# Kernel optimization log

Hardware: AMD Instinct MI355X
Metric: run time of the kernel (lower is better)

Reference implementation:

```python
import jax, jax.numpy as jnp
import numpy as np


def setup_inputs() -> dict:
    key = jax.random.key(0)
    k1, k2 = jax.random.split(key)
    B, S, H = 32, 4096, 1024
    output = jax.random.normal(k1, (B, 1, H), dtype=jnp.float32)
    context = jax.random.normal(k2, (B, S, H), dtype=jnp.float32)
    return {"output": output, "context": context}


def reference(output, context):
    # scores: (B, 1, S) = q @ k^T
    attn = jnp.einsum('bqh,bsh->bqs', output, context)
    attn = jax.nn.softmax(attn, axis=2)
    # out: (B, 1, H) = attn @ context, then tanh
    out = jnp.tanh(jnp.einsum('bqs,bsh->bqh', attn, context))
    return (out, attn)
```

## Files before the change

kernel.cpp:

```cpp
#include <hip/hip_runtime.h>
#include <math.h>

constexpr int kB  = 32;
constexpr int kS  = 4096;
constexpr int kH  = 1024;
constexpr int kNC = 128;
constexpr int kCH = kS / kNC;
constexpr int WPB = 4;
constexpr int NP  = kCH / 2;

#define GLOAD_LDS16(gp, lp)                                                        \
  __builtin_amdgcn_global_load_lds(                                               \
      (const __attribute__((address_space(1))) void*)(gp),                        \
      (__attribute__((address_space(3))) void*)(lp), 16, 0, 0)

__device__ __forceinline__ void stage_row(const float* __restrict__ g,
                                          float* l, int lane) {
  #pragma unroll
  for (int j = 0; j < 4; ++j)
    GLOAD_LDS16(g + j * 256 + 4 * lane, l + j * 256);
}

#define PAIR4(acc4, w04, w14) \
  acc4.x = fmaf(p1, w14.x, fmaf(p0, w04.x, acc4.x * sc)); \
  acc4.y = fmaf(p1, w14.y, fmaf(p0, w04.y, acc4.y * sc)); \
  acc4.z = fmaf(p1, w14.z, fmaf(p0, w04.z, acc4.z * sc)); \
  acc4.w = fmaf(p1, w14.w, fmaf(p0, w04.w, acc4.w * sc));

__global__ __launch_bounds__(256, 2) void attn_pass1(
    const float* __restrict__ q,
    const float* __restrict__ ctx,
    float* __restrict__ scores,
    float* __restrict__ pm,
    float* __restrict__ pl,
    float* __restrict__ pacc)
{
  __shared__ __align__(16) float lds[WPB * 2 * 2048];

  const int lane = threadIdx.x & 63;
  const int wid  = threadIdx.x >> 6;
  const int wave = blockIdx.x * WPB + wid;
  const int b    = wave / kNC;
  const int c    = wave % kNC;

  float* wbuf = &lds[wid * 4096];

  const float4* qp = reinterpret_cast<const float4*>(q + (size_t)b * kH) + lane;
  const float4 Qa = qp[0], Qb = qp[64], Qc = qp[128], Qd = qp[192];

  const float* cbase = ctx + ((size_t)b * kS + (size_t)c * kCH) * kH;

  float m = -3.0e38f, l = 0.0f;
  float4 aa = make_float4(0.f,0.f,0.f,0.f), ab = aa, ac = aa, ad = aa;
  float myscore = 0.0f;

  stage_row(cbase,        wbuf,        lane);
  stage_row(cbase + 1024, wbuf + 1024, lane);

  auto compute_pair = [&](int t) {
    const float4* p0 = reinterpret_cast<const float4*>(wbuf + (t & 1) * 2048) + lane;
    const float4* p1 = p0 + 256;

    const float4 w0a = p0[0], w0b = p0[64], w0c = p0[128], w0d = p0[192];
    const float4 w1a = p1[0], w1b = p1[64], w1c = p1[128], w1d = p1[192];

    float d0, d1;
    d0  = w0a.x*Qa.x + w0a.y*Qa.y + w0a.z*Qa.z + w0a.w*Qa.w;
    d0 += w0b.x*Qb.x + w0b.y*Qb.y + w0b.z*Qb.z + w0b.w*Qb.w;
    d0 += w0c.x*Qc.x + w0c.y*Qc.y + w0c.z*Qc.z + w0c.w*Qc.w;
    d0 += w0d.x*Qd.x + w0d.y*Qd.y + w0d.z*Qd.z + w0d.w*Qd.w;
    d1  = w1a.x*Qa.x + w1a.y*Qa.y + w1a.z*Qa.z + w1a.w*Qa.w;
    d1 += w1b.x*Qb.x + w1b.y*Qb.y + w1b.z*Qb.z + w1b.w*Qb.w;
    d1 += w1c.x*Qc.x + w1c.y*Qc.y + w1c.z*Qc.z + w1c.w*Qc.w;
    d1 += w1d.x*Qd.x + w1d.y*Qd.y + w1d.z*Qd.z + w1d.w*Qd.w;

    #pragma unroll
    for (int off = 32; off >= 1; off >>= 1) {
      d0 += __shfl_xor(d0, off, 64);
      d1 += __shfl_xor(d1, off, 64);
    }

    if (lane == 2 * t)     myscore = d0;
    if (lane == 2 * t + 1) myscore = d1;

    const float nm = fmaxf(m, fmaxf(d0, d1));
    const float sc = __expf(m - nm);
    const float p0s = __expf(d0 - nm);
    const float p1s = __expf(d1 - nm);
    m = nm;
    l = fmaf(l, sc, p0s + p1s);
    { const float p0 = p0s, p1 = p1s;
      PAIR4(aa, w0a, w1a); PAIR4(ab, w0b, w1b);
      PAIR4(ac, w0c, w1c); PAIR4(ad, w0d, w1d); }
  };

  for (int t = 0; t < NP - 1; ++t) {
    const float* g   = cbase + (size_t)(t + 1) * 2048;
    float*       lb  = wbuf + ((t + 1) & 1) * 2048;
    stage_row(g,        lb,        lane);
    stage_row(g + 1024, lb + 1024, lane);
    asm volatile("s_waitcnt vmcnt(8)" ::: "memory");
    compute_pair(t);
  }
  asm volatile("s_waitcnt vmcnt(0)" ::: "memory");
  compute_pair(NP - 1);

  if (lane < kCH) scores[(size_t)b * kS + (size_t)c * kCH + lane] = myscore;
  if (lane == 0) { pm[wave] = m; pl[wave] = l; }
  float4* pap = reinterpret_cast<float4*>(pacc + (size_t)wave * kH) + lane;
  pap[0] = aa; pap[64] = ab; pap[128] = ac; pap[192] = ad;
}

__global__ __launch_bounds__(256) void attn_pass2(
    const float* __restrict__ scores,
    const float* __restrict__ pm,
    const float* __restrict__ pl,
    const float* __restrict__ pacc,
    float* __restrict__ out)
{
  const int b  = blockIdx.x;
  const int by = blockIdx.y;
  const int t  = threadIdx.x;

  __shared__ float red[256];
  __shared__ float wgt[kNC];
  __shared__ float4 sh4[8][32];

  const float mi = (t < kNC) ? pm[b * kNC + t] : -3.0e38f;
  red[t] = mi;
  __syncthreads();
  #pragma unroll
  for (int o = 128; o >= 1; o >>= 1) {
    if (t < o) red[t] = fmaxf(red[t], red[t + o]);
    __syncthreads();
  }
  const float m_g = red[0];
  __syncthreads();

  float li = 0.0f;
  if (t < kNC) {
    const float wi = __expf(mi - m_g);
    wgt[t] = wi;
    li = pl[b * kNC + t] * wi;
  }
  red[t] = li;
  __syncthreads();
  #pragma unroll
  for (int o = 128; o >= 1; o >>= 1) {
    if (t < o) red[t] += red[t + o];
    __syncthreads();
  }
  const float inv = 1.0f / red[0];
  __syncthreads();

  if (by < 8) {
    const int h4     = t & 31;
    const int stripe = t >> 5;
    const float4* base =
        reinterpret_cast<const float4*>(pacc + ((size_t)(b * kNC + stripe)) * kH + by * 128) + h4;
    const size_t istep = (size_t)8 * (kH / 4);

    float4 s = make_float4(0.f, 0.f, 0.f, 0.f);
    #pragma unroll 16
    for (int k = 0; k < 16; ++k) {
      const float w = wgt[stripe + 8 * k];
      const float4 v = base[(size_t)k * istep];
      s.x = fmaf(w, v.x, s.x); s.y = fmaf(w, v.y, s.y);
      s.z = fmaf(w, v.z, s.z); s.w = fmaf(w, v.w, s.w);
    }
    sh4[stripe][h4] = s;
    __syncthreads();

    if (t < 32) {
      float4 r = sh4[0][t];
      #pragma unroll
      for (int i = 1; i < 8; ++i) {
        const float4 v = sh4[i][t];
        r.x += v.x; r.y += v.y; r.z += v.z; r.w += v.w;
      }
      r.x = tanhf(r.x * inv); r.y = tanhf(r.y * inv);
      r.z = tanhf(r.z * inv); r.w = tanhf(r.w * inv);
      reinterpret_cast<float4*>(out + (size_t)b * kH + by * 128)[t] = r;
    }
  } else {
    const float4* sb = reinterpret_cast<const float4*>(scores + (size_t)b * kS);
    float4* ab = reinterpret_cast<float4*>(out + (size_t)kB * kH + (size_t)b * kS);
    #pragma unroll
    for (int k = 0; k < kS / 4 / 256; ++k) {
      const int i = k * 256 + t;
      float4 v = sb[i];
      v.x = __expf(v.x - m_g) * inv; v.y = __expf(v.y - m_g) * inv;
      v.z = __expf(v.z - m_g) * inv; v.w = __expf(v.w - m_g) * inv;
      ab[i] = v;
    }
  }
}

extern "C" void kernel_launch(void* const* d_in, const int* in_sizes, int n_in,
                              void* d_out, int out_size, void* d_ws, size_t ws_size,
                              hipStream_t stream) {
  const float* q   = (const float*)d_in[0];
  const float* ctx = (const float*)d_in[1];
  float* out = (float*)d_out;
  float* ws  = (float*)d_ws;

  float* scores = ws;
  float* pm     = scores + (size_t)kB * kS;
  float* pl     = pm + kB * kNC;
  float* pacc   = pl + kB * kNC;

  attn_pass1<<<dim3(kB * kNC / WPB), 256, 0, stream>>>(q, ctx, scores, pm, pl, pacc);
  attn_pass2<<<dim3(kB, 9), 256, 0, stream>>>(scores, pm, pl, pacc, out);
}
```

Measured before the change: 115.2 us.

## Triple-buffer LDS staging in pass1 and split softmax stats into separate kernel

Pass1 now uses three LDS buffers per wave and keeps two row-pairs in flight, prefetching two steps ahead instead of one. Blocks shrink to two waves of 128 threads, so more workgroups are scheduled per CU while LDS per wave grows. The pass-2 reduction of per-chunk max and sum moves into a small stats kernel that writes normalized weights. The combine kernel then skips the redundant per-block reductions, at the cost of one more kernel launch.

```diff
diff --git a/kernel.cpp b/kernel.cpp
--- a/kernel.cpp
+++ b/kernel.cpp
@@ -6,18 +6,19 @@
 constexpr int kH  = 1024;
 constexpr int kNC = 128;
 constexpr int kCH = kS / kNC;
-constexpr int WPB = 4;
+constexpr int WPB = 2;
 constexpr int NP  = kCH / 2;
+constexpr int NBUF = 3;
 
 #define GLOAD_LDS16(gp, lp)                                                        \
   __builtin_amdgcn_global_load_lds(                                               \
       (const __attribute__((address_space(1))) void*)(gp),                        \
       (__attribute__((address_space(3))) void*)(lp), 16, 0, 0)
 
-__device__ __forceinline__ void stage_row(const float* __restrict__ g,
-                                          float* l, int lane) {
-  #pragma unroll
-  for (int j = 0; j < 4; ++j)
+__device__ __forceinline__ void stage_pair(const float* __restrict__ g,
+                                           float* l, int lane) {
+  #pragma unroll
+  for (int j = 0; j < 8; ++j)
     GLOAD_LDS16(g + j * 256 + 4 * lane, l + j * 256);
 }
 
@@ -27,7 +28,7 @@
   acc4.z = fmaf(p1, w14.z, fmaf(p0, w04.z, acc4.z * sc)); \
   acc4.w = fmaf(p1, w14.w, fmaf(p0, w04.w, acc4.w * sc));
 
-__global__ __launch_bounds__(256, 2) void attn_pass1(
+__global__ __launch_bounds__(128) void attn_pass1(
     const float* __restrict__ q,
     const float* __restrict__ ctx,
     float* __restrict__ scores,
@@ -35,7 +36,7 @@
     float* __restrict__ pl,
     float* __restrict__ pacc)
 {
-  __shared__ __align__(16) float lds[WPB * 2 * 2048];
+  __shared__ __align__(16) float lds[WPB * NBUF * 2048];
 
   const int lane = threadIdx.x & 63;
   const int wid  = threadIdx.x >> 6;
@@ -43,7 +44,7 @@
   const int b    = wave / kNC;
   const int c    = wave % kNC;
 
-  float* wbuf = &lds[wid * 4096];
+  float* wbuf = &lds[wid * NBUF * 2048];
 
   const float4* qp = reinterpret_cast<const float4*>(q + (size_t)b * kH) + lane;
   const float4 Qa = qp[0], Qb = qp[64], Qc = qp[128], Qd = qp[192];
@@ -54,11 +55,8 @@
   float4 aa = make_float4(0.f,0.f,0.f,0.f), ab = aa, ac = aa, ad = aa;
   float myscore = 0.0f;
 
-  stage_row(cbase,        wbuf,        lane);
-  stage_row(cbase + 1024, wbuf + 1024, lane);
-
-  auto compute_pair = [&](int t) {
-    const float4* p0 = reinterpret_cast<const float4*>(wbuf + (t & 1) * 2048) + lane;
+  auto compute_pair = [&](int t, const float* buf) {
+    const float4* p0 = reinterpret_cast<const float4*>(buf) + lane;
     const float4* p1 = p0 + 256;
 
     const float4 w0a = p0[0], w0b = p0[64], w0c = p0[128], w0d = p0[192];
@@ -94,16 +92,19 @@
       PAIR4(ac, w0c, w1c); PAIR4(ad, w0d, w1d); }
   };
 
-  for (int t = 0; t < NP - 1; ++t) {
-    const float* g   = cbase + (size_t)(t + 1) * 2048;
-    float*       lb  = wbuf + ((t + 1) & 1) * 2048;
-    stage_row(g,        lb,        lane);
-    stage_row(g + 1024, lb + 1024, lane);
-    asm volatile("s_waitcnt vmcnt(8)" ::: "memory");
-    compute_pair(t);
-  }
+  stage_pair(cbase + 0 * 2048, wbuf + 0 * 2048, lane);
+  stage_pair(cbase + 1 * 2048, wbuf + 1 * 2048, lane);
+
+  #pragma unroll
+  for (int t = 0; t < NP - 2; ++t) {
+    stage_pair(cbase + (size_t)(t + 2) * 2048, wbuf + ((t + 2) % NBUF) * 2048, lane);
+    asm volatile("s_waitcnt vmcnt(16)" ::: "memory");
+    compute_pair(t, wbuf + (t % NBUF) * 2048);
+  }
+  asm volatile("s_waitcnt vmcnt(8)" ::: "memory");
+  compute_pair(NP - 2, wbuf + ((NP - 2) % NBUF) * 2048);
   asm volatile("s_waitcnt vmcnt(0)" ::: "memory");
-  compute_pair(NP - 1);
+  compute_pair(NP - 1, wbuf + ((NP - 1) % NBUF) * 2048);
 
   if (lane < kCH) scores[(size_t)b * kS + (size_t)c * kCH + lane] = myscore;
   if (lane == 0) { pm[wave] = m; pl[wave] = l; }
@@ -111,10 +112,45 @@
   pap[0] = aa; pap[64] = ab; pap[128] = ac; pap[192] = ad;
 }
 
-__global__ __launch_bounds__(256) void attn_pass2(
-    const float* __restrict__ scores,
+__global__ __launch_bounds__(128) void attn_stats(
     const float* __restrict__ pm,
     const float* __restrict__ pl,
+    float* __restrict__ wgl,
+    float2* __restrict__ stats)
+{
+  const int b = blockIdx.x;
+  const int t = threadIdx.x;
+  __shared__ float red[128];
+
+  const float mi = pm[b * kNC + t];
+  red[t] = mi;
+  __syncthreads();
+  #pragma unroll
+  for (int o = 64; o >= 1; o >>= 1) {
+    if (t < o) red[t] = fmaxf(red[t], red[t + o]);
+    __syncthreads();
+  }
+  const float m_g = red[0];
+  __syncthreads();
+
+  const float wi = __expf(mi - m_g);
+  red[t] = pl[b * kNC + t] * wi;
+  __syncthreads();
+  #pragma unroll
+  for (int o = 64; o >= 1; o >>= 1) {
+    if (t < o) red[t] += red[t + o];
+    __syncthreads();
+  }
+  const float inv = 1.0f / red[0];
+
+  wgl[b * kNC + t] = wi * inv;
+  if (t == 0) stats[b] = make_float2(m_g, inv);
+}
+
+__global__ __launch_bounds__(256) void attn_combine(
+    const float* __restrict__ scores,
+    const float* __restrict__ wgl,
+    const float2* __restrict__ stats,
     const float* __restrict__ pacc,
     float* __restrict__ out)
 {
@@ -122,38 +158,12 @@
   const int by = blockIdx.y;
   const int t  = threadIdx.x;
 
-  __shared__ float red[256];
-  __shared__ float wgt[kNC];
-  __shared__ float4 sh4[8][32];
-
-  const float mi = (t < kNC) ? pm[b * kNC + t] : -3.0e38f;
-  red[t] = mi;
-  __syncthreads();
-  #pragma unroll
-  for (int o = 128; o >= 1; o >>= 1) {
-    if (t < o) red[t] = fmaxf(red[t], red[t + o]);
-    __syncthreads();
-  }
-  const float m_g = red[0];
-  __syncthreads();
-
-  float li = 0.0f;
-  if (t < kNC) {
-    const float wi = __expf(mi - m_g);
-    wgt[t] = wi;
-    li = pl[b * kNC + t] * wi;
-  }
-  red[t] = li;
-  __syncthreads();
-  #pragma unroll
-  for (int o = 128; o >= 1; o >>= 1) {
-    if (t < o) red[t] += red[t + o];
-    __syncthreads();
-  }
-  const float inv = 1.0f / red[0];
-  __syncthreads();
-
   if (by < 8) {
+    __shared__ float wsh[kNC];
+    __shared__ float4 sh4[8][32];
+    if (t < kNC) wsh[t] = wgl[b * kNC + t];
+    __syncthreads();
+
     const int h4     = t & 31;
     const int stripe = t >> 5;
     const float4* base =
@@ -163,7 +173,7 @@
     float4 s = make_float4(0.f, 0.f, 0.f, 0.f);
     #pragma unroll 16
     for (int k = 0; k < 16; ++k) {
-      const float w = wgt[stripe + 8 * k];
+      const float w = wsh[stripe + 8 * k];
       const float4 v = base[(size_t)k * istep];
       s.x = fmaf(w, v.x, s.x); s.y = fmaf(w, v.y, s.y);
       s.z = fmaf(w, v.z, s.z); s.w = fmaf(w, v.w, s.w);
@@ -178,20 +188,22 @@
         const float4 v = sh4[i][t];
         r.x += v.x; r.y += v.y; r.z += v.z; r.w += v.w;
       }
-      r.x = tanhf(r.x * inv); r.y = tanhf(r.y * inv);
-      r.z = tanhf(r.z * inv); r.w = tanhf(r.w * inv);
+      r.x = tanhf(r.x); r.y = tanhf(r.y);
+      r.z = tanhf(r.z); r.w = tanhf(r.w);
       reinterpret_cast<float4*>(out + (size_t)b * kH + by * 128)[t] = r;
     }
   } else {
+    const float2 st = stats[b];
+    const float m_g = st.x, inv = st.y;
     const float4* sb = reinterpret_cast<const float4*>(scores + (size_t)b * kS);
-    float4* ab = reinterpret_cast<float4*>(out + (size_t)kB * kH + (size_t)b * kS);
+    float4* abuf = reinterpret_cast<float4*>(out + (size_t)kB * kH + (size_t)b * kS);
     #pragma unroll
     for (int k = 0; k < kS / 4 / 256; ++k) {
       const int i = k * 256 + t;
       float4 v = sb[i];
       v.x = __expf(v.x - m_g) * inv; v.y = __expf(v.y - m_g) * inv;
       v.z = __expf(v.z - m_g) * inv; v.w = __expf(v.w - m_g) * inv;
-      ab[i] = v;
+      abuf[i] = v;
     }
   }
 }
@@ -207,8 +219,11 @@
   float* scores = ws;
   float* pm     = scores + (size_t)kB * kS;
   float* pl     = pm + kB * kNC;
-  float* pacc   = pl + kB * kNC;
-
-  attn_pass1<<<dim3(kB * kNC / WPB), 256, 0, stream>>>(q, ctx, scores, pm, pl, pacc);
-  attn_pass2<<<dim3(kB, 9), 256, 0, stream>>>(scores, pm, pl, pacc, out);
-}
+  float* wgl    = pl + kB * kNC;
+  float* statsf = wgl + kB * kNC;
+  float* pacc   = statsf + 2 * kB + 32;
+
+  attn_pass1<<<dim3(kB * kNC / WPB), 128, 0, stream>>>(q, ctx, scores, pm, pl, pacc);
+  attn_stats<<<dim3(kB), 128, 0, stream>>>(pm, pl, wgl, (float2*)statsf);
+  attn_combine<<<dim3(kB, 9), 256, 0, stream>>>(scores, wgl, (float2*)statsf, pacc, out);
+}
```

Measured after the change: 181.2 us. 1.57x slower.
